# Performance work log

Measured on AMD Instinct MI355X. Metric: run time of the kernel, lower is better.

## Reference

```python
import jax, jax.numpy as jnp
import numpy as np

MARGIN = 0.3
N_CLASSES = 1024
N_SAMPLES = 32
D = 512


def setup_inputs() -> dict:
    key = jax.random.key(0)
    k1, k2 = jax.random.split(key)
    embeddings = jax.random.normal(k1, (2 * N_CLASSES * N_SAMPLES, D), dtype=jnp.float32)
    target = jax.random.randint(k2, (2 * N_CLASSES * N_SAMPLES,), 0, N_CLASSES, dtype=jnp.int64)
    return {"embeddings": embeddings, "target": target}


def reference(embeddings, target):
    # [C, 2, S, D]: per class, block 0 = positives, block 1 = negatives
    e = embeddings.reshape(N_CLASSES, 2, N_SAMPLES, D)
    pos = e[:, 0]  # [C, S, D]
    neg = e[:, 1]  # [C, S, D]
    anchor = pos.mean(axis=1, keepdims=True)  # [C, 1, D]
    ap = jnp.sum((anchor - pos) ** 2, axis=-1)  # [C, S]
    neg_d = jnp.sum((neg - anchor) ** 2, axis=-1)  # [C, S]
    # an_distances = dist(anchor, nearest negative) == min over negatives
    an = jnp.min(neg_d, axis=1, keepdims=True)  # [C, 1]
    losses = jnp.sum(jax.nn.relu(ap - an + MARGIN), axis=1)  # [C]
    return losses.mean()
```

## Files before the change

### kernel.cpp

```cpp
#include <hip/hip_runtime.h>

#define NC 1024
#define NS 32
#define DD 512
#define MARGIN 0.3f

__global__ __launch_bounds__(256) void ccl_per_class(const float* __restrict__ emb,
                                                     float* __restrict__ class_loss) {
    const int c = blockIdx.x;
    const int t = threadIdx.x;
    const int g = t >> 7;
    const int col4 = t & 127;
    const float4* posv = (const float4*)(emb + (size_t)c * (2 * NS * DD));
    const float4* negv = posv + NS * DD / 4;

    __shared__ float4 s_part[2][128];
    __shared__ float4 s_anchor[128];
    __shared__ float s_wap[4][16];
    __shared__ float s_wnd[4][16];

    float4 p[16], n[16];
#pragma unroll
    for (int j = 0; j < 16; ++j) p[j] = posv[(2 * j + g) * (DD / 4) + col4];
#pragma unroll
    for (int j = 0; j < 16; ++j) n[j] = negv[(2 * j + g) * (DD / 4) + col4];

    float4 acc = p[0];
#pragma unroll
    for (int j = 1; j < 16; ++j) {
        acc.x += p[j].x; acc.y += p[j].y; acc.z += p[j].z; acc.w += p[j].w;
    }
    s_part[g][col4] = acc;
    __syncthreads();
    if (t < 128) {
        float4 a = s_part[0][t];
        float4 b = s_part[1][t];
        a.x = (a.x + b.x) * (1.f / NS);
        a.y = (a.y + b.y) * (1.f / NS);
        a.z = (a.z + b.z) * (1.f / NS);
        a.w = (a.w + b.w) * (1.f / NS);
        s_anchor[t] = a;
    }
    __syncthreads();

    const float4 a = s_anchor[col4];
    float apc[16], ndc[16];
#pragma unroll
    for (int j = 0; j < 16; ++j) {
        float dx = p[j].x - a.x, dy = p[j].y - a.y, dz = p[j].z - a.z, dw = p[j].w - a.w;
        apc[j] = dx * dx + dy * dy + dz * dz + dw * dw;
        dx = n[j].x - a.x; dy = n[j].y - a.y; dz = n[j].z - a.z; dw = n[j].w - a.w;
        ndc[j] = dx * dx + dy * dy + dz * dz + dw * dw;
    }

#pragma unroll
    for (int m = 1; m < 64; m <<= 1) {
#pragma unroll
        for (int j = 0; j < 16; ++j) {
            apc[j] += __shfl_xor(apc[j], m);
            ndc[j] += __shfl_xor(ndc[j], m);
        }
    }
    const int wv = t >> 6;
    if ((t & 63) == 0) {
#pragma unroll
        for (int j = 0; j < 16; ++j) { s_wap[wv][j] = apc[j]; s_wnd[wv][j] = ndc[j]; }
    }
    __syncthreads();

    if (t < NS) {
        const int sg = t & 1, sj = t >> 1;
        float ap = s_wap[2 * sg][sj] + s_wap[2 * sg + 1][sj];
        float nd = s_wnd[2 * sg][sj] + s_wnd[2 * sg + 1][sj];
        float an = nd;
#pragma unroll
        for (int m = 1; m < 32; m <<= 1) an = fminf(an, __shfl_xor(an, m));
        float l = fmaxf(ap - an + MARGIN, 0.f);
#pragma unroll
        for (int m = 1; m < 32; m <<= 1) l += __shfl_xor(l, m);
        if (t == 0) class_loss[c] = l;
    }
}

__global__ __launch_bounds__(256) void ccl_reduce(const float* __restrict__ class_loss,
                                                  float* __restrict__ out) {
    const int t = threadIdx.x;
    float v = class_loss[t] + class_loss[t + 256] + class_loss[t + 512] + class_loss[t + 768];
#pragma unroll
    for (int m = 32; m >= 1; m >>= 1) v += __shfl_down(v, m);
    __shared__ float s_partial[4];
    if ((t & 63) == 0) s_partial[t >> 6] = v;
    __syncthreads();
    if (t == 0)
        out[0] = (s_partial[0] + s_partial[1] + s_partial[2] + s_partial[3]) * (1.f / NC);
}

extern "C" void kernel_launch(void* const* d_in, const int* in_sizes, int n_in,
                              void* d_out, int out_size, void* d_ws, size_t ws_size,
                              hipStream_t stream) {
    const float* emb = (const float*)d_in[0];
    float* cls = (float*)d_ws;
    float* out = (float*)d_out;
    ccl_per_class<<<NC, 256, 0, stream>>>(emb, cls);
    ccl_reduce<<<1, 256, 0, stream>>>(cls, out);
}
```

Measured before the change: 29.61 us.

## Fuse final reduction via last-block atomic counter, widen blocks, transpose-reduce columns

Merges the per-class and final mean kernels into one launch: each block publishes its class loss and bumps an atomic counter, and the last block to finish sums all class losses. Blocks grow to 512 threads so each thread holds half as many rows in registers. The per-row wave reduction is replaced by a butterfly transpose-reduce that needs fewer shuffles, and the separate anchor-broadcast sync is removed. It adds a memset launch for the counter and an atomic handoff that depends on correct acquire/release ordering.

```diff
diff --git a/kernel.cpp b/kernel.cpp
--- a/kernel.cpp
+++ b/kernel.cpp
@@ -5,71 +5,87 @@
 #define DD 512
 #define MARGIN 0.3f
 
-__global__ __launch_bounds__(256) void ccl_per_class(const float* __restrict__ emb,
-                                                     float* __restrict__ class_loss) {
+__device__ __forceinline__ float reduce_cols8(float v[8], int lane) {
+#pragma unroll
+    for (int m = 1, len = 8; m <= 4; m <<= 1, len >>= 1) {
+        const int half = len >> 1;
+#pragma unroll
+        for (int i = 0; i < half; ++i) {
+            float lo = v[i], hi = v[i + half];
+            float send = (lane & m) ? lo : hi;
+            float recv = __shfl_xor(send, m);
+            v[i] = (lane & m) ? (hi + recv) : (lo + recv);
+        }
+    }
+    float r = v[0];
+    r += __shfl_xor(r, 8);
+    r += __shfl_xor(r, 16);
+    r += __shfl_xor(r, 32);
+    return r;
+}
+
+__global__ __launch_bounds__(512) void ccl_fused(const float* __restrict__ emb,
+                                                 float* __restrict__ cls,
+                                                 unsigned* __restrict__ cnt,
+                                                 float* __restrict__ out) {
     const int c = blockIdx.x;
     const int t = threadIdx.x;
     const int g = t >> 7;
     const int col4 = t & 127;
+    const int lane = t & 63;
+    const int wv = t >> 6;
     const float4* posv = (const float4*)(emb + (size_t)c * (2 * NS * DD));
     const float4* negv = posv + NS * DD / 4;
 
-    __shared__ float4 s_part[2][128];
-    __shared__ float4 s_anchor[128];
-    __shared__ float s_wap[4][16];
-    __shared__ float s_wnd[4][16];
+    __shared__ float4 s_part[4][128];
+    __shared__ float s_wap[8][8];
+    __shared__ float s_wnd[8][8];
+    __shared__ float s_fin[8];
+    __shared__ unsigned s_old;
 
-    float4 p[16], n[16];
+    float4 p[8], n[8];
 #pragma unroll
-    for (int j = 0; j < 16; ++j) p[j] = posv[(2 * j + g) * (DD / 4) + col4];
+    for (int j = 0; j < 8; ++j) p[j] = posv[(4 * j + g) * (DD / 4) + col4];
 #pragma unroll
-    for (int j = 0; j < 16; ++j) n[j] = negv[(2 * j + g) * (DD / 4) + col4];
+    for (int j = 0; j < 8; ++j) n[j] = negv[(4 * j + g) * (DD / 4) + col4];
 
     float4 acc = p[0];
 #pragma unroll
-    for (int j = 1; j < 16; ++j) {
+    for (int j = 1; j < 8; ++j) {
         acc.x += p[j].x; acc.y += p[j].y; acc.z += p[j].z; acc.w += p[j].w;
     }
     s_part[g][col4] = acc;
     __syncthreads();
-    if (t < 128) {
-        float4 a = s_part[0][t];
-        float4 b = s_part[1][t];
-        a.x = (a.x + b.x) * (1.f / NS);
-        a.y = (a.y + b.y) * (1.f / NS);
-        a.z = (a.z + b.z) * (1.f / NS);
-        a.w = (a.w + b.w) * (1.f / NS);
-        s_anchor[t] = a;
+    float4 a;
+    {
+        float4 x0 = s_part[0][col4], x1 = s_part[1][col4];
+        float4 x2 = s_part[2][col4], x3 = s_part[3][col4];
+        a.x = (x0.x + x1.x + x2.x + x3.x) * (1.f / NS);
+        a.y = (x0.y + x1.y + x2.y + x3.y) * (1.f / NS);
+        a.z = (x0.z + x1.z + x2.z + x3.z) * (1.f / NS);
+        a.w = (x0.w + x1.w + x2.w + x3.w) * (1.f / NS);
     }
-    __syncthreads();
 
-    const float4 a = s_anchor[col4];
-    float apc[16], ndc[16];
+    float apc[8], ndc[8];
 #pragma unroll
-    for (int j = 0; j < 16; ++j) {
+    for (int j = 0; j < 8; ++j) {
         float dx = p[j].x - a.x, dy = p[j].y - a.y, dz = p[j].z - a.z, dw = p[j].w - a.w;
         apc[j] = dx * dx + dy * dy + dz * dz + dw * dw;
         dx = n[j].x - a.x; dy = n[j].y - a.y; dz = n[j].z - a.z; dw = n[j].w - a.w;
         ndc[j] = dx * dx + dy * dy + dz * dz + dw * dw;
     }
 
-#pragma unroll
-    for (int m = 1; m < 64; m <<= 1) {
-#pragma unroll
-        for (int j = 0; j < 16; ++j) {
-            apc[j] += __shfl_xor(apc[j], m);
-            ndc[j] += __shfl_xor(ndc[j], m);
-        }
-    }
-    const int wv = t >> 6;
-    if ((t & 63) == 0) {
-#pragma unroll
-        for (int j = 0; j < 16; ++j) { s_wap[wv][j] = apc[j]; s_wnd[wv][j] = ndc[j]; }
+    float rap = reduce_cols8(apc, lane);
+    float rnd = reduce_cols8(ndc, lane);
+    if (lane < 8) {
+        const int jm = ((lane & 1) << 2) | (lane & 2) | ((lane & 4) >> 2);
+        s_wap[wv][jm] = rap;
+        s_wnd[wv][jm] = rnd;
     }
     __syncthreads();
 
     if (t < NS) {
-        const int sg = t & 1, sj = t >> 1;
+        const int sg = t & 3, sj = t >> 2;
         float ap = s_wap[2 * sg][sj] + s_wap[2 * sg + 1][sj];
         float nd = s_wnd[2 * sg][sj] + s_wnd[2 * sg + 1][sj];
         float an = nd;
@@ -78,29 +94,36 @@
         float l = fmaxf(ap - an + MARGIN, 0.f);
 #pragma unroll
         for (int m = 1; m < 32; m <<= 1) l += __shfl_xor(l, m);
-        if (t == 0) class_loss[c] = l;
+        if (t == 0) {
+            __hip_atomic_store(&cls[c], l, __ATOMIC_RELAXED, __HIP_MEMORY_SCOPE_AGENT);
+            s_old = __hip_atomic_fetch_add(cnt, 1u, __ATOMIC_ACQ_REL, __HIP_MEMORY_SCOPE_AGENT);
+        }
     }
-}
+    __syncthreads();
 
-__global__ __launch_bounds__(256) void ccl_reduce(const float* __restrict__ class_loss,
-                                                  float* __restrict__ out) {
-    const int t = threadIdx.x;
-    float v = class_loss[t] + class_loss[t + 256] + class_loss[t + 512] + class_loss[t + 768];
+    if (s_old == NC - 1) {
+        float v = __hip_atomic_load(&cls[t], __ATOMIC_ACQUIRE, __HIP_MEMORY_SCOPE_AGENT) +
+                  __hip_atomic_load(&cls[t + 512], __ATOMIC_ACQUIRE, __HIP_MEMORY_SCOPE_AGENT);
 #pragma unroll
-    for (int m = 32; m >= 1; m >>= 1) v += __shfl_down(v, m);
-    __shared__ float s_partial[4];
-    if ((t & 63) == 0) s_partial[t >> 6] = v;
-    __syncthreads();
-    if (t == 0)
-        out[0] = (s_partial[0] + s_partial[1] + s_partial[2] + s_partial[3]) * (1.f / NC);
+        for (int m = 1; m < 64; m <<= 1) v += __shfl_xor(v, m);
+        if (lane == 0) s_fin[wv] = v;
+        __syncthreads();
+        if (t == 0) {
+            float tot = 0.f;
+#pragma unroll
+            for (int w = 0; w < 8; ++w) tot += s_fin[w];
+            out[0] = tot * (1.f / NC);
+        }
+    }
 }
 
 extern "C" void kernel_launch(void* const* d_in, const int* in_sizes, int n_in,
                               void* d_out, int out_size, void* d_ws, size_t ws_size,
                               hipStream_t stream) {
     const float* emb = (const float*)d_in[0];
-    float* cls = (float*)d_ws;
+    unsigned* cnt = (unsigned*)d_ws;
+    float* cls = (float*)((char*)d_ws + 256);
     float* out = (float*)d_out;
-    ccl_per_class<<<NC, 256, 0, stream>>>(emb, cls);
-    ccl_reduce<<<1, 256, 0, stream>>>(cls, out);
+    hipMemsetAsync(cnt, 0, 4, stream);
+    ccl_fused<<<NC, 512, 0, stream>>>(emb, cls, cnt, out);
 }
```

Result: slower. 61.47 us (+107.6%).

## Use one column per thread and butterfly transpose-reduce for per-sample distances

Applied to the files above, without the earlier changes.

Each block now runs 512 threads, and each thread owns one embedding column for all 32 positives and 32 negatives. This lets the anchor mean be computed in registers with no shared-memory pass and no barriers. The per-sample wave reductions use a butterfly that halves the active array at each shuffle step, which cuts the shuffle count from 6*32 to about 31+1 per array. The trade-offs are scalar instead of float4 loads, though each wave still reads 256 B contiguous, and more waves per block.

```diff
diff --git a/kernel.cpp b/kernel.cpp
--- a/kernel.cpp
+++ b/kernel.cpp
@@ -5,80 +5,68 @@
 #define DD 512
 #define MARGIN 0.3f
 
-__global__ __launch_bounds__(256) void ccl_per_class(const float* __restrict__ emb,
-                                                     float* __restrict__ class_loss) {
+__global__ __launch_bounds__(512) void ccl_per_class(const float* __restrict__ emb,
+                                                     float* __restrict__ cls) {
     const int c = blockIdx.x;
     const int t = threadIdx.x;
-    const int g = t >> 7;
-    const int col4 = t & 127;
-    const float4* posv = (const float4*)(emb + (size_t)c * (2 * NS * DD));
-    const float4* negv = posv + NS * DD / 4;
+    const int lane = t & 63;
+    const int wv = t >> 6;
+    const float* pos = emb + (size_t)c * (2 * NS * DD);
+    const float* neg = pos + NS * DD;
 
-    __shared__ float4 s_part[2][128];
-    __shared__ float4 s_anchor[128];
-    __shared__ float s_wap[4][16];
-    __shared__ float s_wnd[4][16];
+    __shared__ float s_wap[8][32];
+    __shared__ float s_wnd[8][32];
 
-    float4 p[16], n[16];
+    float p[32], n[32];
 #pragma unroll
-    for (int j = 0; j < 16; ++j) p[j] = posv[(2 * j + g) * (DD / 4) + col4];
+    for (int s = 0; s < 32; ++s) p[s] = pos[s * DD + t];
 #pragma unroll
-    for (int j = 0; j < 16; ++j) n[j] = negv[(2 * j + g) * (DD / 4) + col4];
+    for (int s = 0; s < 32; ++s) n[s] = neg[s * DD + t];
 
-    float4 acc = p[0];
+    float a = 0.f;
 #pragma unroll
-    for (int j = 1; j < 16; ++j) {
-        acc.x += p[j].x; acc.y += p[j].y; acc.z += p[j].z; acc.w += p[j].w;
-    }
-    s_part[g][col4] = acc;
-    __syncthreads();
-    if (t < 128) {
-        float4 a = s_part[0][t];
-        float4 b = s_part[1][t];
-        a.x = (a.x + b.x) * (1.f / NS);
-        a.y = (a.y + b.y) * (1.f / NS);
-        a.z = (a.z + b.z) * (1.f / NS);
-        a.w = (a.w + b.w) * (1.f / NS);
-        s_anchor[t] = a;
-    }
-    __syncthreads();
-
-    const float4 a = s_anchor[col4];
-    float apc[16], ndc[16];
-#pragma unroll
-    for (int j = 0; j < 16; ++j) {
-        float dx = p[j].x - a.x, dy = p[j].y - a.y, dz = p[j].z - a.z, dw = p[j].w - a.w;
-        apc[j] = dx * dx + dy * dy + dz * dz + dw * dw;
-        dx = n[j].x - a.x; dy = n[j].y - a.y; dz = n[j].z - a.z; dw = n[j].w - a.w;
-        ndc[j] = dx * dx + dy * dy + dz * dz + dw * dw;
-    }
+    for (int s = 0; s < 32; ++s) a += p[s];
+    a *= (1.f / NS);
 
 #pragma unroll
-    for (int m = 1; m < 64; m <<= 1) {
+    for (int s = 0; s < 32; ++s) { float d = p[s] - a; p[s] = d * d; }
 #pragma unroll
-        for (int j = 0; j < 16; ++j) {
-            apc[j] += __shfl_xor(apc[j], m);
-            ndc[j] += __shfl_xor(ndc[j], m);
-        }
+    for (int s = 0; s < 32; ++s) { float d = n[s] - a; n[s] = d * d; }
+
+#define BSTEP(arr, m, half)                                        \
+    {                                                              \
+        _Pragma("unroll")                                          \
+        for (int i = 0; i < (half); ++i) {                         \
+            float lo = arr[i], hi = arr[i + (half)];               \
+            float send = (lane & (m)) ? lo : hi;                   \
+            float recv = __shfl_xor(send, (m));                    \
+            arr[i] = (lane & (m)) ? (hi + recv) : (lo + recv);     \
+        }                                                          \
     }
-    const int wv = t >> 6;
-    if ((t & 63) == 0) {
-#pragma unroll
-        for (int j = 0; j < 16; ++j) { s_wap[wv][j] = apc[j]; s_wnd[wv][j] = ndc[j]; }
+    BSTEP(p, 1, 16) BSTEP(p, 2, 8) BSTEP(p, 4, 4) BSTEP(p, 8, 2) BSTEP(p, 16, 1)
+    BSTEP(n, 1, 16) BSTEP(n, 2, 8) BSTEP(n, 4, 4) BSTEP(n, 8, 2) BSTEP(n, 16, 1)
+#undef BSTEP
+    float rap = p[0] + __shfl_xor(p[0], 32);
+    float rnd = n[0] + __shfl_xor(n[0], 32);
+    if (lane < 32) {
+        const int jm = ((lane & 1) << 4) | ((lane & 2) << 2) | (lane & 4) |
+                       ((lane & 8) >> 2) | ((lane & 16) >> 4);
+        s_wap[wv][jm] = rap;
+        s_wnd[wv][jm] = rnd;
     }
     __syncthreads();
 
     if (t < NS) {
-        const int sg = t & 1, sj = t >> 1;
-        float ap = s_wap[2 * sg][sj] + s_wap[2 * sg + 1][sj];
-        float nd = s_wnd[2 * sg][sj] + s_wnd[2 * sg + 1][sj];
+        float ap = 0.f, nd = 0.f;
+#pragma unroll
+        for (int w = 0; w < 8; ++w) { ap += s_wap[w][t]; nd += s_wnd[w][t]; }
         float an = nd;
 #pragma unroll
         for (int m = 1; m < 32; m <<= 1) an = fminf(an, __shfl_xor(an, m));
         float l = fmaxf(ap - an + MARGIN, 0.f);
 #pragma unroll
         for (int m = 1; m < 32; m <<= 1) l += __shfl_xor(l, m);
-        if (t == 0) class_loss[c] = l;
+        if (t == 0) cls[c] = l;
     }
 }
 
@@ -101,6 +89,6 @@
     const float* emb = (const float*)d_in[0];
     float* cls = (float*)d_ws;
     float* out = (float*)d_out;
-    ccl_per_class<<<NC, 256, 0, stream>>>(emb, cls);
+    ccl_per_class<<<NC, 512, 0, stream>>>(emb, cls);
     ccl_reduce<<<1, 256, 0, stream>>>(cls, out);
 }
```

Result: no change. 29.42 us (-0.7%).
